# Kernel optimization log

Measured on AMD Instinct MI355X. Metric: run time of the kernel, lower is better.

The kernel has to match this reference:

```python
import jax, jax.numpy as jnp
import numpy as np

N_HEADS = 16
N_EMBED = 1024
HEAD_DIM = N_EMBED // N_HEADS
B, T = 4, 2048


def setup_inputs() -> dict:
    key = jax.random.key(0)
    k1, k2, k3 = jax.random.split(key, 3)
    scale = 1.0 / np.sqrt(N_EMBED)
    x = jax.random.normal(k1, (B, T, N_EMBED), dtype=jnp.float32)
    w_qkv = jax.random.normal(k2, (N_EMBED, 3 * N_EMBED), dtype=jnp.float32) * scale
    w_out = jax.random.normal(k3, (N_EMBED, N_EMBED), dtype=jnp.float32) * scale
    b_out = jnp.zeros((N_EMBED,), dtype=jnp.float32)
    return {"x": x, "w_qkv": w_qkv, "w_out": w_out, "b_out": b_out}


def reference(x, w_qkv, w_out, b_out):
    b, t, c = x.shape
    # qkv projection (no bias), split into q,k,v per head: [B, H, T, D]
    qkv = (x @ w_qkv).reshape(b, t, 3, N_HEADS, HEAD_DIM)
    q, k, v = jnp.moveaxis(qkv, 2, 0)            # each [B, T, H, D]
    q = jnp.swapaxes(q, 1, 2) * (HEAD_DIM ** -0.5)  # [B, H, T, D]
    k = jnp.swapaxes(k, 1, 2)
    v = jnpp = jnp.swapaxes(v, 1, 2)
    # scores + causal mask
    attn = jnp.einsum('bhqd,bhkd->bhqk', q, k)   # [B, H, T, T]
    causal = jnp.tril(jnp.ones((t, t), dtype=bool))
    attn = jnp.where(causal, attn, -jnp.inf)
    attn = jax.nn.softmax(attn, axis=-1)
    out = jnp.einsum('bhqk,bhkd->bhqd', attn, v)  # [B, H, T, D]
    out = jnp.swapaxes(out, 1, 2).reshape(b, t, c)
    # output projection (dropout is identity in eval mode)
    return out @ w_out + b_out
```

## Files before the change

### kernel.cpp

```cpp
#include <hip/hip_runtime.h>

#define NH 16
#define HD 64
#define CE 1024
#define TT 2048
#define BB 4
#define MM 8192

using bf16x8 = __attribute__((ext_vector_type(8))) __bf16;
using f32x4  = __attribute__((ext_vector_type(4))) float;
using f32x16 = __attribute__((ext_vector_type(16))) float;

__device__ __forceinline__ unsigned short f2bf(float f) {
  unsigned int u = __float_as_uint(f);
  u += 0x7fffu + ((u >> 16) & 1u);
  return (unsigned short)(u >> 16);
}

__device__ __forceinline__ unsigned cvtpk(float lo, float hi) {
  unsigned r;
  asm("v_cvt_pk_bf16_f32 %0, %1, %2" : "=v"(r) : "v"(lo), "v"(hi));
  return r;
}

__device__ __forceinline__ void async_cp16(const unsigned short* g, unsigned short* l) {
  __builtin_amdgcn_global_load_lds(
      (const __attribute__((address_space(1))) unsigned int*)g,
      (__attribute__((address_space(3))) unsigned int*)l, 16, 0, 0);
}

__global__ __launch_bounds__(256) void prep(const float* __restrict__ x,
                                            const float* __restrict__ w_qkv,
                                            const float* __restrict__ w_out,
                                            unsigned short* __restrict__ Xb,
                                            unsigned short* __restrict__ Wt1,
                                            unsigned short* __restrict__ Wt2) {
  __shared__ unsigned short tile[32][33];
  const int idx = blockIdx.x;
  if (idx < 8192) {
    const int i = (idx * 256 + threadIdx.x) * 4;
    const float4 v = *(const float4*)(x + i);
    ushort4 o;
    o.x = f2bf(v.x); o.y = f2bf(v.y); o.z = f2bf(v.z); o.w = f2bf(v.w);
    *(ushort4*)(Xb + i) = o;
    return;
  }
  const float* in;
  unsigned short* out;
  int rows, cols, bx, by;
  if (idx < 11264) {
    const int tc = idx - 8192;
    in = w_qkv; out = Wt1; rows = 1024; cols = 3072;
    bx = tc % 96; by = tc / 96;
  } else {
    const int tc = idx - 11264;
    in = w_out; out = Wt2; rows = 1024; cols = 1024;
    bx = tc & 31; by = tc >> 5;
  }
  const int c0 = bx * 32, r0 = by * 32;
  const int tx = threadIdx.x & 31, ty = threadIdx.x >> 5;
#pragma unroll
  for (int i = ty; i < 32; i += 8)
    tile[i][tx] = f2bf(in[(size_t)(r0 + i) * cols + c0 + tx]);
  __syncthreads();
#pragma unroll
  for (int i = ty; i < 32; i += 8)
    out[(size_t)(c0 + i) * rows + r0 + tx] = tile[tx][i];
}

__device__ __forceinline__ void gemm_core(const unsigned short* __restrict__ A,
                                          const unsigned short* __restrict__ BT,
                                          int m0, int n0, f32x4 (&acc)[4][4],
                                          unsigned short* As, unsigned short* Bs) {
  const int tid  = threadIdx.x;
  const int lane = tid & 63;
  const int wave = tid >> 6;
  const int quad = lane >> 4;
  const int l15  = lane & 15;
  const int wm = (wave & 1) * 64;
  const int wn = (wave >> 1) * 64;
  const int ldr = tid >> 2;
  const int ldc = (tid & 3) * 8;
  const unsigned short* Ap = A + (size_t)(m0 + ldr) * CE + ldc;
  const unsigned short* Bp = BT + (size_t)(n0 + ldr) * CE + ldc;
  const int wofs = wave * 512;
#define STAGE_K(buf, k0)                                                   \
  do {                                                                     \
    async_cp16(Ap + (k0), As + (buf) * 4096 + wofs);                       \
    async_cp16(Ap + (size_t)64 * CE + (k0), As + (buf) * 4096 + 2048 + wofs); \
    async_cp16(Bp + (k0), Bs + (buf) * 4096 + wofs);                       \
    async_cp16(Bp + (size_t)64 * CE + (k0), Bs + (buf) * 4096 + 2048 + wofs); \
  } while (0)
  STAGE_K(0, 0);
  __syncthreads();
  int cur = 0;
  for (int k0 = 0; k0 < CE; k0 += 32) {
    if (k0 + 32 < CE) STAGE_K(cur ^ 1, k0 + 32);
    const unsigned short* Ab = As + cur * 4096;
    const unsigned short* Bb = Bs + cur * 4096;
    bf16x8 af[4], bfr[4];
#pragma unroll
    for (int i = 0; i < 4; i++) {
      af[i]  = *(const bf16x8*)&Ab[(wm + i * 16 + l15) * 32 + quad * 8];
      bfr[i] = *(const bf16x8*)&Bb[(wn + i * 16 + l15) * 32 + quad * 8];
    }
    __builtin_amdgcn_s_setprio(1);
#pragma unroll
    for (int mi = 0; mi < 4; mi++)
#pragma unroll
      for (int ni = 0; ni < 4; ni++)
        acc[mi][ni] = __builtin_amdgcn_mfma_f32_16x16x32_bf16(af[mi], bfr[ni], acc[mi][ni], 0, 0, 0);
    __builtin_amdgcn_s_setprio(0);
    __syncthreads();
    cur ^= 1;
  }
#undef STAGE_K
}

__global__ __launch_bounds__(256) void gemm_qkv(const unsigned short* __restrict__ A,
                                                const unsigned short* __restrict__ BT,
                                                unsigned short* __restrict__ Qb,
                                                unsigned short* __restrict__ Kb,
                                                unsigned short* __restrict__ Vtb) {
  __shared__ unsigned short pool[16384];
  f32x4 acc[4][4] = {};
  const int m0 = blockIdx.y * 128, n0 = blockIdx.x * 128;
  gemm_core(A, BT, m0, n0, acc, pool, pool + 8192);
  const int tid = threadIdx.x, lane = tid & 63, wave = tid >> 6;
  const int quad = lane >> 4, l15 = lane & 15;
  const int wm = (wave & 1) * 64, wn = (wave >> 1) * 64;
  if (blockIdx.x >= 16) {
    unsigned short* Vt = pool;
    const int h0 = 2 * (blockIdx.x - 16);
    const int bb = m0 >> 11;
    const int t0g = m0 & 2047;
    const int l31 = tid & 31;
    const int rw  = tid >> 5;
    unsigned int* __restrict__ VtU = (unsigned int*)Vtb;
#pragma unroll
    for (int hp = 0; hp < 2; hp++) {
      __syncthreads();
      if ((wave & 1) == hp) {
#pragma unroll
        for (int mi = 0; mi < 4; mi++)
#pragma unroll
          for (int ni = 0; ni < 4; ni++) {
            const int row = wn + ni * 16 + l15;
            const int col = mi * 16 + quad * 4;
#pragma unroll
            for (int r = 0; r < 4; r++)
              Vt[row * 66 + col + r] = f2bf(acc[mi][ni][r]);
          }
      }
      __syncthreads();
#pragma unroll
      for (int k = 0; k < 16; k++) {
        const int d = rw + 8 * k;
        const unsigned int v = *(const unsigned int*)&Vt[d * 66 + 2 * l31];
        const int hh = h0 + (d >> 6);
        VtU[((((size_t)(bb * 16 + hh) * 64 + (d & 63)) * TT + t0g + 64 * hp) >> 1) + l31] = v;
      }
    }
    return;
  }
  const float QSCALE = 0.125f * 1.44269504088896340736f;
#pragma unroll
  for (int mi = 0; mi < 4; mi++) {
#pragma unroll
    for (int ni = 0; ni < 4; ni++) {
      const int n = n0 + wn + ni * 16 + l15;
      const int s = n >> 10;
      const int h = (n >> 6) & 15;
      const int d = n & 63;
#pragma unroll
      for (int r = 0; r < 4; r++) {
        const int m = m0 + wm + mi * 16 + quad * 4 + r;
        const int b = m >> 11;
        const int t = m & 2047;
        const int bh = (b << 4) + h;
        const float v = acc[mi][ni][r];
        if (s == 0) Qb[((size_t)bh * TT + t) * HD + d] = f2bf(v * QSCALE);
        else        Kb[((size_t)bh * TT + t) * HD + d] = f2bf(v);
      }
    }
  }
}

__global__ __launch_bounds__(256) void gemm_out(const unsigned short* __restrict__ A,
                                                const unsigned short* __restrict__ BT,
                                                const float* __restrict__ bias,
                                                float* __restrict__ out) {
  __shared__ unsigned short pool[16384];
  f32x4 acc[4][4] = {};
  const int m0 = blockIdx.y * 128, n0 = blockIdx.x * 128;
  gemm_core(A, BT, m0, n0, acc, pool, pool + 8192);
  const int tid = threadIdx.x, lane = tid & 63, wave = tid >> 6;
  const int quad = lane >> 4, l15 = lane & 15;
  const int wm = (wave & 1) * 64, wn = (wave >> 1) * 64;
#pragma unroll
  for (int mi = 0; mi < 4; mi++) {
#pragma unroll
    for (int ni = 0; ni < 4; ni++) {
      const int n = n0 + wn + ni * 16 + l15;
      const float bv = bias[n];
#pragma unroll
      for (int r = 0; r < 4; r++) {
        const int m = m0 + wm + mi * 16 + quad * 4 + r;
        out[(size_t)m * CE + n] = acc[mi][ni][r] + bv;
      }
    }
  }
}

__global__ __launch_bounds__(256) void flash_attn(const unsigned short* __restrict__ Q,
                                                  const unsigned short* __restrict__ Kg,
                                                  const unsigned short* __restrict__ Vt,
                                                  unsigned short* __restrict__ AO) {
  __shared__ unsigned short Ks[64][72];
  __shared__ unsigned short Vs[64][72];
  const int flat = blockIdx.x + 8 * blockIdx.y;
  const int wu   = (flat & 7) * 64 + (flat >> 3);
  const int qx   = wu & 7;
  const int bh   = wu >> 3;
  const int tid = threadIdx.x, w = tid >> 6, lane = tid & 63;
  const int l31 = lane & 31, hi = lane >> 5;
  const int b = bh >> 4, h = bh & 15;
  const unsigned short* Kbase = Kg + (size_t)bh * TT * HD;
  const unsigned short* Vbase = Vt + (size_t)bh * HD * TT;
  const int srow = tid >> 2;
  const int scol = (tid & 3) * 16;
  const bf16x8 ones = {1, 1, 1, 1, 1, 1, 1, 1};

  for (int ph = 0; ph < 2; ph++) {
    const int pt = ph ? (15 - qx) : qx;
    const int q0 = pt * 128;
    const int n_it = 2 * pt + 2;
    const int wr = q0 + w * 32;
    bf16x8 qf[4];
#pragma unroll
    for (int ds_ = 0; ds_ < 4; ds_++)
      qf[ds_] = *(const bf16x8*)(Q + ((size_t)bh * TT + wr + l31) * HD + ds_ * 16 + hi * 8);
    f32x16 o0 = {}, o1 = {}, l_acc = {};
    uint4 kreg[2], vreg[2];
    {
      const unsigned short* kp = Kbase + (size_t)srow * HD + scol;
      kreg[0] = *(const uint4*)kp;
      kreg[1] = *(const uint4*)(kp + 8);
      const unsigned short* vp = Vbase + (size_t)srow * TT + scol;
      vreg[0] = *(const uint4*)vp;
      vreg[1] = *(const uint4*)(vp + 8);
    }
    for (int it = 0; it < n_it; it++) {
      const int kv0 = it * 64;
      *(uint4*)&Ks[srow][scol]     = kreg[0];
      *(uint4*)&Ks[srow][scol + 8] = kreg[1];
      *(uint4*)&Vs[srow][scol]     = vreg[0];
      *(uint4*)&Vs[srow][scol + 8] = vreg[1];
      {
        const int itn = (it + 1 < n_it) ? it + 1 : it;
        const int kvn = itn * 64;
        const unsigned short* kp = Kbase + (size_t)(kvn + srow) * HD + scol;
        kreg[0] = *(const uint4*)kp;
        kreg[1] = *(const uint4*)(kp + 8);
        const unsigned short* vp = Vbase + (size_t)srow * TT + kvn + scol;
        vreg[0] = *(const uint4*)vp;
        vreg[1] = *(const uint4*)(vp + 8);
      }
      __syncthreads();
      if (kv0 <= wr + 31) {
        const int qg = wr + l31;
#pragma unroll
        for (int kt = 0; kt < 2; kt++) {
          f32x16 sc = {};
          __builtin_amdgcn_s_setprio(1);
#pragma unroll
          for (int ds_ = 0; ds_ < 4; ds_++) {
            const bf16x8 kb = *(const bf16x8*)&Ks[kt * 32 + l31][ds_ * 16 + hi * 8];
            sc = __builtin_amdgcn_mfma_f32_32x32x16_bf16(kb, qf[ds_], sc, 0, 0, 0);
          }
          __builtin_amdgcn_s_setprio(0);
          float p[16];
          const int kvb = kv0 + kt * 32 + 4 * hi;
          if (kv0 + 63 > wr) {
#pragma unroll
            for (int r = 0; r < 16; r++) {
              const int kvg = kvb + (r & 3) + 8 * (r >> 2);
              p[r] = exp2f(kvg <= qg ? sc[r] : -1e30f);
            }
          } else {
#pragma unroll
            for (int r = 0; r < 16; r++) p[r] = exp2f(sc[r]);
          }
          bf16x8 pa[2];
#pragma unroll
          for (int sl = 0; sl < 2; sl++) {
            unsigned a0 = cvtpk(p[8 * sl + 0], p[8 * sl + 1]);
            unsigned a1 = cvtpk(p[8 * sl + 2], p[8 * sl + 3]);
            unsigned a2 = cvtpk(p[8 * sl + 4], p[8 * sl + 5]);
            unsigned a3 = cvtpk(p[8 * sl + 6], p[8 * sl + 7]);
            asm volatile("v_permlane32_swap_b32 %0, %1" : "+v"(a0), "+v"(a2));
            asm volatile("v_permlane32_swap_b32 %0, %1" : "+v"(a1), "+v"(a3));
            union { unsigned u[4]; bf16x8 v; } c;
            c.u[0] = a0; c.u[1] = a1; c.u[2] = a2; c.u[3] = a3;
            pa[sl] = c.v;
          }
          __builtin_amdgcn_s_setprio(1);
          l_acc = __builtin_amdgcn_mfma_f32_32x32x16_bf16(pa[0], ones, l_acc, 0, 0, 0);
          l_acc = __builtin_amdgcn_mfma_f32_32x32x16_bf16(pa[1], ones, l_acc, 0, 0, 0);
#pragma unroll
          for (int sl = 0; sl < 2; sl++) {
            const bf16x8 vb0 = *(const bf16x8*)&Vs[l31][kt * 32 + sl * 16 + hi * 8];
            const bf16x8 vb1 = *(const bf16x8*)&Vs[32 + l31][kt * 32 + sl * 16 + hi * 8];
            o0 = __builtin_amdgcn_mfma_f32_32x32x16_bf16(pa[sl], vb0, o0, 0, 0, 0);
            o1 = __builtin_amdgcn_mfma_f32_32x32x16_bf16(pa[sl], vb1, o1, 0, 0, 0);
          }
          __builtin_amdgcn_s_setprio(0);
        }
      }
      __syncthreads();
    }
    {
      float rin[16];
#pragma unroll
      for (int r = 0; r < 16; r++) rin[r] = __builtin_amdgcn_rcpf(l_acc[r]);
#pragma unroll
      for (int r = 0; r < 16; r++) {
        const int row_g = wr + (r & 3) + 8 * (r >> 2) + 4 * hi;
        const size_t base = ((size_t)b * TT + row_g) * CE + h * 64;
        AO[base + l31]      = f2bf(o0[r] * rin[r]);
        AO[base + 32 + l31] = f2bf(o1[r] * rin[r]);
      }
    }
  }
}

extern "C" void kernel_launch(void* const* d_in, const int* in_sizes, int n_in,
                              void* d_out, int out_size, void* d_ws, size_t ws_size,
                              hipStream_t stream) {
  const float* x     = (const float*)d_in[0];
  const float* w_qkv = (const float*)d_in[1];
  const float* w_out = (const float*)d_in[2];
  const float* b_out = (const float*)d_in[3];
  float* out = (float*)d_out;

  unsigned short* ws  = (unsigned short*)d_ws;
  unsigned short* Xb  = ws;
  unsigned short* Wt1 = Xb  + (size_t)MM * CE;
  unsigned short* Wt2 = Wt1 + (size_t)3072 * 1024;
  unsigned short* Qb  = Wt2 + (size_t)1024 * 1024;
  unsigned short* Kb  = Qb  + (size_t)8388608;
  unsigned short* Vtb = Kb  + (size_t)8388608;
  unsigned short* AO  = Vtb + (size_t)8388608;

  prep      <<<dim3(12288), 256, 0, stream>>>(x, w_qkv, w_out, Xb, Wt1, Wt2);
  gemm_qkv  <<<dim3(24, 64), 256, 0, stream>>>(Xb, Wt1, Qb, Kb, Vtb);
  flash_attn<<<dim3(8, 64), 256, 0, stream>>>(Qb, Kb, Vtb, AO);
  gemm_out  <<<dim3(8, 64), 256, 0, stream>>>(AO, Wt2, b_out, out);
}
```

Baseline: 287.4 us.

## Split attention KV tile across two wave groups with shared-memory reduction

The flash attention block goes from 256 to 512 threads. Each pair of waves shares one 32-row query slice, and each wave in the pair handles one 32-key half of every 64-key tile. Partial O and row-sum accumulators are then combined through shared memory before normalization. This doubles the waves available per block to hide latency and halves the per-wave serial chain, at the cost of an extra LDS reduction, extra syncs and a larger shared-memory footprint. Softmax uses no running max, so summing partials is valid.

New measurement: 257.2 us. 10.5% less time.

```diff
diff --git a/kernel.cpp b/kernel.cpp
--- a/kernel.cpp
+++ b/kernel.cpp
@@ -212,114 +212,127 @@
   }
 }
 
-__global__ __launch_bounds__(256) void flash_attn(const unsigned short* __restrict__ Q,
+__global__ __launch_bounds__(512) void flash_attn(const unsigned short* __restrict__ Q,
                                                   const unsigned short* __restrict__ Kg,
                                                   const unsigned short* __restrict__ Vt,
                                                   unsigned short* __restrict__ AO) {
-  __shared__ unsigned short Ks[64][72];
-  __shared__ unsigned short Vs[64][72];
+  __shared__ __align__(16) unsigned char smem[49152];
+  unsigned short (*Ks)[72] = (unsigned short (*)[72])smem;
+  unsigned short (*Vs)[72] = (unsigned short (*)[72])(smem + 9216);
+  float4* Sc = (float4*)smem;
   const int flat = blockIdx.x + 8 * blockIdx.y;
   const int wu   = (flat & 7) * 64 + (flat >> 3);
   const int qx   = wu & 7;
   const int bh   = wu >> 3;
   const int tid = threadIdx.x, w = tid >> 6, lane = tid & 63;
   const int l31 = lane & 31, hi = lane >> 5;
+  const int w2 = w & 3, hi2 = w >> 2;
   const int b = bh >> 4, h = bh & 15;
   const unsigned short* Kbase = Kg + (size_t)bh * TT * HD;
   const unsigned short* Vbase = Vt + (size_t)bh * HD * TT;
-  const int srow = tid >> 2;
-  const int scol = (tid & 3) * 16;
+  const int srow = tid >> 3;
+  const int scol = (tid & 7) * 8;
   const bf16x8 ones = {1, 1, 1, 1, 1, 1, 1, 1};
+  union V16 { f32x16 v; float4 c[4]; };
 
   for (int ph = 0; ph < 2; ph++) {
     const int pt = ph ? (15 - qx) : qx;
     const int q0 = pt * 128;
     const int n_it = 2 * pt + 2;
-    const int wr = q0 + w * 32;
+    const int wr = q0 + w2 * 32;
     bf16x8 qf[4];
 #pragma unroll
     for (int ds_ = 0; ds_ < 4; ds_++)
       qf[ds_] = *(const bf16x8*)(Q + ((size_t)bh * TT + wr + l31) * HD + ds_ * 16 + hi * 8);
     f32x16 o0 = {}, o1 = {}, l_acc = {};
-    uint4 kreg[2], vreg[2];
-    {
-      const unsigned short* kp = Kbase + (size_t)srow * HD + scol;
-      kreg[0] = *(const uint4*)kp;
-      kreg[1] = *(const uint4*)(kp + 8);
-      const unsigned short* vp = Vbase + (size_t)srow * TT + scol;
-      vreg[0] = *(const uint4*)vp;
-      vreg[1] = *(const uint4*)(vp + 8);
-    }
+    uint4 kreg, vreg;
+    kreg = *(const uint4*)(Kbase + (size_t)srow * HD + scol);
+    vreg = *(const uint4*)(Vbase + (size_t)srow * TT + scol);
     for (int it = 0; it < n_it; it++) {
       const int kv0 = it * 64;
-      *(uint4*)&Ks[srow][scol]     = kreg[0];
-      *(uint4*)&Ks[srow][scol + 8] = kreg[1];
-      *(uint4*)&Vs[srow][scol]     = vreg[0];
-      *(uint4*)&Vs[srow][scol + 8] = vreg[1];
+      *(uint4*)&Ks[srow][scol] = kreg;
+      *(uint4*)&Vs[srow][scol] = vreg;
       {
         const int itn = (it + 1 < n_it) ? it + 1 : it;
         const int kvn = itn * 64;
-        const unsigned short* kp = Kbase + (size_t)(kvn + srow) * HD + scol;
-        kreg[0] = *(const uint4*)kp;
-        kreg[1] = *(const uint4*)(kp + 8);
-        const unsigned short* vp = Vbase + (size_t)srow * TT + kvn + scol;
-        vreg[0] = *(const uint4*)vp;
-        vreg[1] = *(const uint4*)(vp + 8);
+        kreg = *(const uint4*)(Kbase + (size_t)(kvn + srow) * HD + scol);
+        vreg = *(const uint4*)(Vbase + (size_t)srow * TT + kvn + scol);
       }
       __syncthreads();
-      if (kv0 <= wr + 31) {
+      const int kvs = kv0 + hi2 * 32;
+      if (kvs <= wr + 31) {
+        f32x16 sc = {};
+        __builtin_amdgcn_s_setprio(1);
+#pragma unroll
+        for (int ds_ = 0; ds_ < 4; ds_++) {
+          const bf16x8 kb = *(const bf16x8*)&Ks[hi2 * 32 + l31][ds_ * 16 + hi * 8];
+          sc = __builtin_amdgcn_mfma_f32_32x32x16_bf16(kb, qf[ds_], sc, 0, 0, 0);
+        }
+        __builtin_amdgcn_s_setprio(0);
+        float p[16];
         const int qg = wr + l31;
-#pragma unroll
-        for (int kt = 0; kt < 2; kt++) {
-          f32x16 sc = {};
-          __builtin_amdgcn_s_setprio(1);
-#pragma unroll
-          for (int ds_ = 0; ds_ < 4; ds_++) {
-            const bf16x8 kb = *(const bf16x8*)&Ks[kt * 32 + l31][ds_ * 16 + hi * 8];
-            sc = __builtin_amdgcn_mfma_f32_32x32x16_bf16(kb, qf[ds_], sc, 0, 0, 0);
+        const int kvb = kvs + 4 * hi;
+        if (kvs + 31 > wr) {
+#pragma unroll
+          for (int r = 0; r < 16; r++) {
+            const int kvg = kvb + (r & 3) + 8 * (r >> 2);
+            p[r] = exp2f(kvg <= qg ? sc[r] : -1e30f);
           }
-          __builtin_amdgcn_s_setprio(0);
-          float p[16];
-          const int kvb = kv0 + kt * 32 + 4 * hi;
-          if (kv0 + 63 > wr) {
-#pragma unroll
-            for (int r = 0; r < 16; r++) {
-              const int kvg = kvb + (r & 3) + 8 * (r >> 2);
-              p[r] = exp2f(kvg <= qg ? sc[r] : -1e30f);
-            }
-          } else {
-#pragma unroll
-            for (int r = 0; r < 16; r++) p[r] = exp2f(sc[r]);
-          }
-          bf16x8 pa[2];
-#pragma unroll
-          for (int sl = 0; sl < 2; sl++) {
-            unsigned a0 = cvtpk(p[8 * sl + 0], p[8 * sl + 1]);
-            unsigned a1 = cvtpk(p[8 * sl + 2], p[8 * sl + 3]);
-            unsigned a2 = cvtpk(p[8 * sl + 4], p[8 * sl + 5]);
-            unsigned a3 = cvtpk(p[8 * sl + 6], p[8 * sl + 7]);
-            asm volatile("v_permlane32_swap_b32 %0, %1" : "+v"(a0), "+v"(a2));
-            asm volatile("v_permlane32_swap_b32 %0, %1" : "+v"(a1), "+v"(a3));
-            union { unsigned u[4]; bf16x8 v; } c;
-            c.u[0] = a0; c.u[1] = a1; c.u[2] = a2; c.u[3] = a3;
-            pa[sl] = c.v;
-          }
-          __builtin_amdgcn_s_setprio(1);
-          l_acc = __builtin_amdgcn_mfma_f32_32x32x16_bf16(pa[0], ones, l_acc, 0, 0, 0);
-          l_acc = __builtin_amdgcn_mfma_f32_32x32x16_bf16(pa[1], ones, l_acc, 0, 0, 0);
-#pragma unroll
-          for (int sl = 0; sl < 2; sl++) {
-            const bf16x8 vb0 = *(const bf16x8*)&Vs[l31][kt * 32 + sl * 16 + hi * 8];
-            const bf16x8 vb1 = *(const bf16x8*)&Vs[32 + l31][kt * 32 + sl * 16 + hi * 8];
-            o0 = __builtin_amdgcn_mfma_f32_32x32x16_bf16(pa[sl], vb0, o0, 0, 0, 0);
-            o1 = __builtin_amdgcn_mfma_f32_32x32x16_bf16(pa[sl], vb1, o1, 0, 0, 0);
-          }
-          __builtin_amdgcn_s_setprio(0);
+        } else {
+#pragma unroll
+          for (int r = 0; r < 16; r++) p[r] = exp2f(sc[r]);
         }
+        bf16x8 pa[2];
+#pragma unroll
+        for (int sl = 0; sl < 2; sl++) {
+          unsigned a0 = cvtpk(p[8 * sl + 0], p[8 * sl + 1]);
+          unsigned a1 = cvtpk(p[8 * sl + 2], p[8 * sl + 3]);
+          unsigned a2 = cvtpk(p[8 * sl + 4], p[8 * sl + 5]);
+          unsigned a3 = cvtpk(p[8 * sl + 6], p[8 * sl + 7]);
+          asm volatile("v_permlane32_swap_b32 %0, %1" : "+v"(a0), "+v"(a2));
+          asm volatile("v_permlane32_swap_b32 %0, %1" : "+v"(a1), "+v"(a3));
+          union { unsigned u[4]; bf16x8 v; } c;
+          c.u[0] = a0; c.u[1] = a1; c.u[2] = a2; c.u[3] = a3;
+          pa[sl] = c.v;
+        }
+        __builtin_amdgcn_s_setprio(1);
+        l_acc = __builtin_amdgcn_mfma_f32_32x32x16_bf16(pa[0], ones, l_acc, 0, 0, 0);
+        l_acc = __builtin_amdgcn_mfma_f32_32x32x16_bf16(pa[1], ones, l_acc, 0, 0, 0);
+#pragma unroll
+        for (int sl = 0; sl < 2; sl++) {
+          const bf16x8 vb0 = *(const bf16x8*)&Vs[l31][hi2 * 32 + sl * 16 + hi * 8];
+          const bf16x8 vb1 = *(const bf16x8*)&Vs[32 + l31][hi2 * 32 + sl * 16 + hi * 8];
+          o0 = __builtin_amdgcn_mfma_f32_32x32x16_bf16(pa[sl], vb0, o0, 0, 0, 0);
+          o1 = __builtin_amdgcn_mfma_f32_32x32x16_bf16(pa[sl], vb1, o1, 0, 0, 0);
+        }
+        __builtin_amdgcn_s_setprio(0);
       }
       __syncthreads();
     }
-    {
+    if (hi2) {
+      V16 a;
+      a.v = o0;
+#pragma unroll
+      for (int c = 0; c < 4; c++) Sc[(w2 * 12 + c) * 64 + lane] = a.c[c];
+      a.v = o1;
+#pragma unroll
+      for (int c = 0; c < 4; c++) Sc[(w2 * 12 + 4 + c) * 64 + lane] = a.c[c];
+      a.v = l_acc;
+#pragma unroll
+      for (int c = 0; c < 4; c++) Sc[(w2 * 12 + 8 + c) * 64 + lane] = a.c[c];
+    }
+    __syncthreads();
+    if (!hi2) {
+      V16 a;
+#pragma unroll
+      for (int c = 0; c < 4; c++) a.c[c] = Sc[(w2 * 12 + c) * 64 + lane];
+      o0 = o0 + a.v;
+#pragma unroll
+      for (int c = 0; c < 4; c++) a.c[c] = Sc[(w2 * 12 + 4 + c) * 64 + lane];
+      o1 = o1 + a.v;
+#pragma unroll
+      for (int c = 0; c < 4; c++) a.c[c] = Sc[(w2 * 12 + 8 + c) * 64 + lane];
+      l_acc = l_acc + a.v;
       float rin[16];
 #pragma unroll
       for (int r = 0; r < 16; r++) rin[r] = __builtin_amdgcn_rcpf(l_acc[r]);
@@ -331,6 +344,7 @@
         AO[base + 32 + l31] = f2bf(o1[r] * rin[r]);
       }
     }
+    __syncthreads();
   }
 }
 
@@ -354,6 +368,6 @@
 
   prep      <<<dim3(12288), 256, 0, stream>>>(x, w_qkv, w_out, Xb, Wt1, Wt2);
   gemm_qkv  <<<dim3(24, 64), 256, 0, stream>>>(Xb, Wt1, Qb, Kb, Vtb);
-  flash_attn<<<dim3(8, 64), 256, 0, stream>>>(Qb, Kb, Vtb, AO);
+  flash_attn<<<dim3(8, 64), 512, 0, stream>>>(Qb, Kb, Vtb, AO);
   gemm_out  <<<dim3(8, 64), 256, 0, stream>>>(AO, Wt2, b_out, out);
 }
```
